# Kernel tuning notes

Hardware: AMD Instinct MI355X
Metric: run time of the kernel (lower is better)

The kernel has to match this reference:

```python
import jax, jax.numpy as jnp
import numpy as np

P = 3          # patch_length
P2 = 9         # patch_length**2
CENTER = 4     # patch_center_idx = P2 // 2
REF_LEN = 1    # reference_patch_length
EPS_SHIFT = 1e-6


def _unfold3(feat):
    # F.unfold(feat, 3, padding=1).view(B, C*9, H, W): channel order c*9 + ki*3 + kj
    B, C, H, W = feat.shape
    p = jnp.pad(feat, ((0, 0), (0, 0), (1, 1), (1, 1)))
    patches = [p[:, :, i:i + H, j:j + W] for i in range(3) for j in range(3)]
    return jnp.stack(patches, axis=2).reshape(B, C * 9, H, W)


def _mlp(x, w0, b0, w1, b1, w2, b2, w3, b3, w4, b4):
    h = jax.nn.relu(x @ w0 + b0)
    h = jax.nn.relu(h @ w1 + b1)
    h = jax.nn.relu(h @ w2 + b2)
    h = jax.nn.relu(h @ w3 + b3)
    return h @ w4 + b4


def _forward(feat, coord, cell, w0, b0, w1, b1, w2, b2, w3, b3, w4, b4):
    B, C, H, W = feat.shape
    Q = coord.shape[1]
    featu = _unfold3(feat)                      # (B, C*9, H, W)
    rx = 1.0 / H                                # 2 / H / 2
    ry = 1.0 / W
    coord_p = coord.reshape(B, Q, P2, 2)        # pairs: [...,0]=h-coord, [...,1]=w-coord
    bidx = jnp.arange(B)[:, None]
    # bug-faithful rel_coord scaling: even indices scaled by H then W, odd never
    rel_scale = jnp.array([float(H) * float(W), 1.0], coord.dtype)
    cell_scale = jnp.array([float(H), float(W)], cell.dtype)
    v_lst = [i for i in range(-REF_LEN, REF_LEN + 1) if i != 0]
    preds, areas = [], []
    for vx in v_lst:
        for vy in v_lst:
            shift = jnp.array([vx * rx + EPS_SHIFT, vy * ry + EPS_SHIFT], coord.dtype)
            center = jnp.clip(coord_p[:, :, CENTER, :] + shift, -1 + 1e-6, 1 - 1e-6)
            # nearest grid_sample, align_corners=False: idx = round((g+1)*size/2 - 0.5)
            row = jnp.clip(jnp.round((center[..., 0] + 1) * H / 2 - 0.5).astype(jnp.int32), 0, H - 1)
            col = jnp.clip(jnp.round((center[..., 1] + 1) * W / 2 - 0.5).astype(jnp.int32), 0, W - 1)
            q_feat = featu[bidx, :, row, col]                       # (B, Q, C*9)
            q_coord = jnp.stack([(2 * row + 1) / H - 1,
                                 (2 * col + 1) / W - 1], -1).astype(coord.dtype)
            rel = (coord_p - q_coord[:, :, None, :]) * rel_scale    # (B, Q, P2, 2)
            rel_flat = rel.reshape(B, Q, 2 * P2)
            rel_cell = cell * cell_scale
            x = jnp.concatenate([q_feat, rel_flat, rel_cell], axis=-1)
            pred = _mlp(x, w0, b0, w1, b1, w2, b2, w3, b3, w4, b4)  # (B, Q, 27)
            preds.append(pred)
            areas.append(jnp.abs(rel[:, :, 0, 0] * rel[:, :, 0, 1]) + 1e-9)
    tot = areas[0] + areas[1] + areas[2] + areas[3]
    # local_ensemble: swap diagonally opposite areas
    areas[0], areas[3] = areas[3], areas[0]
    areas[1], areas[2] = areas[2], areas[1]
    ret = jnp.zeros_like(preds[0])
    for p_, a_ in zip(preds, areas):
        ret = ret + p_ * (a_ / tot)[..., None]
    return ret


def setup_inputs() -> dict:
    key = jax.random.key(0)
    ks = jax.random.split(key, 8)
    B, C, H, W, Q = 8, 64, 48, 48, 8192
    HID, OUT = 256, 27
    in_dim = C * 9 + 2 * P2 + 2  # 596
    feat = jax.random.normal(ks[0], (B, C, H, W), jnp.float32)
    coord = jax.random.uniform(ks[1], (B, Q, 2 * P2), jnp.float32, -1.0, 1.0)
    cell = jnp.full((B, Q, 2), 2.0 / (H * 4), jnp.float32)

    def lin(k, fi, fo):
        return (jax.random.normal(k, (fi, fo), jnp.float32) / np.sqrt(fi)).astype(jnp.float32)

    return {
        'feat': feat, 'coord': coord, 'cell': cell,
        'w0': lin(ks[2], in_dim, HID), 'b0': jnp.zeros((HID,), jnp.float32),
        'w1': lin(ks[3], HID, HID), 'b1': jnp.zeros((HID,), jnp.float32),
        'w2': lin(ks[4], HID, HID), 'b2': jnp.zeros((HID,), jnp.float32),
        'w3': lin(ks[5], HID, HID), 'b3': jnp.zeros((HID,), jnp.float32),
        'w4': lin(ks[6], HID, OUT), 'b4': jnp.zeros((OUT,), jnp.float32),
    }


def reference(feat, coord, cell, w0, b0, w1, b1, w2, b2, w3, b3, w4, b4):
    return _forward(feat, coord, cell, w0, b0, w1, b1, w2, b2, w3, b3, w4, b4)
```

## Files before the change

### kernel.cpp

```cpp
#include <hip/hip_runtime.h>
#include <hip/hip_bf16.h>

typedef _Float16 f16x8 __attribute__((ext_vector_type(8)));
typedef float f32x4 __attribute__((ext_vector_type(4)));

#define BQ 65536
#define KPAD0 640
#define HID 256
#define NOUT 27

__device__ __forceinline__ void gl_lds16(const _Float16* g, _Float16* l) {
    __builtin_amdgcn_global_load_lds(
        (const __attribute__((address_space(1))) void*)g,
        (__attribute__((address_space(3))) void*)l, 16, 0, 0);
}

__global__ __launch_bounds__(256) void feat_transpose(
    const float* __restrict__ feat, _Float16* __restrict__ featT,
    _Float16* __restrict__ zbuf)
{
    __shared__ float tile[64 * 49];
    int bh = blockIdx.x;
    int b = bh / 48, h = bh - b * 48;
    int t = threadIdx.x;
    if (bh == 0 && t < 128) zbuf[t] = (_Float16)0.f;
    #pragma unroll
    for (int i = 0; i < 12; i++) {
        int idx = t + i * 256;
        int c = idx / 48, w = idx - c * 48;
        tile[c * 49 + w] = feat[(((size_t)b * 64 + c) * 48 + h) * 48 + w];
    }
    __syncthreads();
    #pragma unroll
    for (int i = 0; i < 12; i++) {
        int idx = t + i * 256;
        int w = idx >> 6, c = idx & 63;
        featT[(((size_t)b * 48 + h) * 48 + w) * 64 + c] = (_Float16)tile[c * 49 + w];
    }
}

__global__ void transpose_cast(const float* __restrict__ w, _Float16* __restrict__ wt,
                               int Kin, int Nin, int Kpad, int Npad) {
    int idx = blockIdx.x * 256 + threadIdx.x;
    if (idx >= Npad * Kpad) return;
    int n = idx / Kpad, k = idx - n * Kpad;
    float v = (n < Nin && k < Kin) ? w[k * Nin + n] : 0.f;
    wt[idx] = (_Float16)v;
}

__global__ void transpose_cast_w0(const float* __restrict__ w0, _Float16* __restrict__ wt) {
    int idx = blockIdx.x * 256 + threadIdx.x;
    if (idx >= 256 * KPAD0) return;
    int n = idx / KPAD0, kp = idx - n * KPAD0;
    int src = (kp < 576) ? ((kp & 63) * 9 + (kp >> 6)) : kp;
    float v = (src < 596) ? w0[src * 256 + n] : 0.f;
    wt[idx] = (_Float16)v;
}

__global__ __launch_bounds__(256, 2) void mega(
    const _Float16* __restrict__ featT, const float* __restrict__ coord,
    const float* __restrict__ cell, const _Float16* __restrict__ zbuf,
    const _Float16* __restrict__ W0t, const _Float16* __restrict__ W1t,
    const _Float16* __restrict__ W2t, const _Float16* __restrict__ W3t,
    const _Float16* __restrict__ W4t,
    const float* __restrict__ b0, const float* __restrict__ b1,
    const float* __restrict__ b2, const float* __restrict__ b3,
    const float* __restrict__ b4, float* __restrict__ preds)
{
    __shared__ _Float16 act[64 * 256];
    __shared__ _Float16 Bs[256 * 32];
    __shared__ int   rc_s[64][2];
    __shared__ float q_s[64][2];
    __shared__ float wgt[64];

    int t = threadIdx.x;
    int wave = t >> 6, lane = t & 63;
    int lrow = lane & 15, lq = lane >> 4;
    int blk = blockIdx.x;
    int s = blk & 3;
    int bq0 = (blk >> 2) * 64;
    _Float16* As = act;

    if (t < 64) {
        int bq = bq0 + t;
        const float* cp = coord + (size_t)bq * 18;
        float areas[4]; int mri = 0, mci = 0; float mqx = 0.f, mqy = 0.f;
        #pragma unroll
        for (int ss = 0; ss < 4; ss++) {
            float vx = (ss & 2) ? 1.f : -1.f, vy = (ss & 1) ? 1.f : -1.f;
            float cx = cp[8] + vx * (1.f / 48.f) + 1e-6f;
            float cy = cp[9] + vy * (1.f / 48.f) + 1e-6f;
            cx = fminf(fmaxf(cx, -1.f + 1e-6f), 1.f - 1e-6f);
            cy = fminf(fmaxf(cy, -1.f + 1e-6f), 1.f - 1e-6f);
            int ri = (int)rintf((cx + 1.f) * 24.f - 0.5f); ri = min(max(ri, 0), 47);
            int ci = (int)rintf((cy + 1.f) * 24.f - 0.5f); ci = min(max(ci, 0), 47);
            float qx = (float)(2 * ri + 1) / 48.f - 1.f;
            float qy = (float)(2 * ci + 1) / 48.f - 1.f;
            areas[ss] = fabsf((cp[0] - qx) * 2304.f * (cp[1] - qy)) + 1e-9f;
            if (ss == s) { mri = ri; mci = ci; mqx = qx; mqy = qy; }
        }
        float tot = areas[0] + areas[1] + areas[2] + areas[3];
        wgt[t] = areas[s ^ 3] / tot;
        rc_s[t][0] = mri; rc_s[t][1] = mci;
        q_s[t][0] = mqx;  q_s[t][1] = mqy;
    }
    __syncthreads();

    int gdat = (lane & 3) ^ ((lane >> 3) & 3);

    f32x4 acc[4][4];
    #pragma unroll
    for (int mi = 0; mi < 4; mi++)
        #pragma unroll
        for (int ni = 0; ni < 4; ni++) acc[mi][ni] = (f32x4){0.f, 0.f, 0.f, 0.f};

    {
        int srow = wave * 16 + (lane >> 2);
        int sbq  = bq0 + srow;
        int s_ri = rc_s[srow][0], s_ci = rc_s[srow][1];
        const _Float16* fbase = featT + ((size_t)(sbq >> 13)) * (48 * 48 * 64);

        for (int p = 0; p < 9; p++) {
            int di = p / 3 - 1, dj = p - (p / 3) * 3 - 1;
            int r2 = s_ri + di, c2 = s_ci + dj;
            const _Float16* src = ((unsigned)r2 < 48u && (unsigned)c2 < 48u)
                ? fbase + (((size_t)r2 * 48 + c2) << 6) : zbuf;
            #pragma unroll
            for (int half = 0; half < 2; half++) {
                __syncthreads();
                gl_lds16(src + half * 32 + gdat * 8, &As[wave * 512]);
                int k0 = p * 64 + half * 32;
                #pragma unroll
                for (int j = 0; j < 4; j++) {
                    int slab = j * 4 + wave;
                    int br = slab * 16 + (lane >> 2);
                    gl_lds16(W0t + (size_t)br * KPAD0 + k0 + gdat * 8, &Bs[slab * 512]);
                }
                __syncthreads();
                f16x8 af[4], bf[4];
                #pragma unroll
                for (int mi = 0; mi < 4; mi++) {
                    int ar = mi * 16 + lrow;
                    af[mi] = *(const f16x8*)&As[ar * 32 + ((lq ^ ((ar >> 1) & 3)) << 3)];
                }
                #pragma unroll
                for (int ni = 0; ni < 4; ni++) {
                    int br = wave * 64 + ni * 16 + lrow;
                    bf[ni] = *(const f16x8*)&Bs[br * 32 + ((lq ^ ((br >> 1) & 3)) << 3)];
                }
                #pragma unroll
                for (int mi = 0; mi < 4; mi++)
                    #pragma unroll
                    for (int ni = 0; ni < 4; ni++)
                        acc[mi][ni] = __builtin_amdgcn_mfma_f32_16x16x32_f16(
                            af[mi], bf[ni], acc[mi][ni], 0, 0, 0);
            }
        }
        {
            __syncthreads();
            int r = t >> 2, c0 = (t & 3) * 8;
            int bq = bq0 + r;
            const float* cp2 = coord + (size_t)bq * 18;
            float qx = q_s[r][0], qy = q_s[r][1];
            _Float16 tmp[8];
            #pragma unroll
            for (int j = 0; j < 8; j++) {
                int idx = c0 + j;
                float v;
                if (idx < 18) v = (idx & 1) ? (cp2[idx] - qy) : ((cp2[idx] - qx) * 2304.f);
                else if (idx == 18) v = cell[(size_t)bq * 2] * 48.f;
                else if (idx == 19) v = cell[(size_t)bq * 2 + 1] * 48.f;
                else v = 0.f;
                tmp[j] = (_Float16)v;
            }
            int gslot = ((c0 >> 3) ^ ((r >> 1) & 3)) & 3;
            *(int4*)&As[r * 32 + gslot * 8] = *(int4*)&tmp[0];
            #pragma unroll
            for (int j = 0; j < 4; j++) {
                int slab = j * 4 + wave;
                int br = slab * 16 + (lane >> 2);
                gl_lds16(W0t + (size_t)br * KPAD0 + 576 + gdat * 8, &Bs[slab * 512]);
            }
            __syncthreads();
            f16x8 af[4], bf[4];
            #pragma unroll
            for (int mi = 0; mi < 4; mi++) {
                int ar = mi * 16 + lrow;
                af[mi] = *(const f16x8*)&As[ar * 32 + ((lq ^ ((ar >> 1) & 3)) << 3)];
            }
            #pragma unroll
            for (int ni = 0; ni < 4; ni++) {
                int br = wave * 64 + ni * 16 + lrow;
                bf[ni] = *(const f16x8*)&Bs[br * 32 + ((lq ^ ((br >> 1) & 3)) << 3)];
            }
            #pragma unroll
            for (int mi = 0; mi < 4; mi++)
                #pragma unroll
                for (int ni = 0; ni < 4; ni++)
                    acc[mi][ni] = __builtin_amdgcn_mfma_f32_16x16x32_f16(
                        af[mi], bf[ni], acc[mi][ni], 0, 0, 0);
        }
    }
    __syncthreads();
    {
        float bvv[4];
        #pragma unroll
        for (int ni = 0; ni < 4; ni++) bvv[ni] = b0[wave * 64 + ni * 16 + lrow];
        #pragma unroll
        for (int mi = 0; mi < 4; mi++)
            #pragma unroll
            for (int ni = 0; ni < 4; ni++) {
                int cw = wave * 64 + ni * 16 + lrow;
                #pragma unroll
                for (int rr = 0; rr < 4; rr++) {
                    float v = acc[mi][ni][rr] + bvv[ni];
                    v = v > 0.f ? v : 0.f;
                    int rw = mi * 16 + lq * 4 + rr;
                    int gp = ((cw >> 3) ^ (rw & 31)) & 31;
                    act[rw * 256 + gp * 8 + (cw & 7)] = (_Float16)v;
                }
            }
    }

    for (int layer = 0; layer < 3; layer++) {
        const _Float16* Wl = (layer == 0) ? W1t : (layer == 1) ? W2t : W3t;
        const float*    bl = (layer == 0) ? b1  : (layer == 1) ? b2  : b3;
        #pragma unroll
        for (int mi = 0; mi < 4; mi++)
            #pragma unroll
            for (int ni = 0; ni < 4; ni++) acc[mi][ni] = (f32x4){0.f, 0.f, 0.f, 0.f};
        #pragma unroll 2
        for (int k0 = 0; k0 < 256; k0 += 32) {
            __syncthreads();
            #pragma unroll
            for (int j = 0; j < 4; j++) {
                int slab = j * 4 + wave;
                int br = slab * 16 + (lane >> 2);
                gl_lds16(Wl + (size_t)br * 256 + k0 + gdat * 8, &Bs[slab * 512]);
            }
            __syncthreads();
            f16x8 af[4], bf[4];
            #pragma unroll
            for (int mi = 0; mi < 4; mi++) {
                int ar = mi * 16 + lrow;
                int gp = (((k0 >> 3) + lq) ^ (ar & 31)) & 31;
                af[mi] = *(const f16x8*)&act[ar * 256 + gp * 8];
            }
            #pragma unroll
            for (int ni = 0; ni < 4; ni++) {
                int br = wave * 64 + ni * 16 + lrow;
                bf[ni] = *(const f16x8*)&Bs[br * 32 + ((lq ^ ((br >> 1) & 3)) << 3)];
            }
            #pragma unroll
            for (int mi = 0; mi < 4; mi++)
                #pragma unroll
                for (int ni = 0; ni < 4; ni++)
                    acc[mi][ni] = __builtin_amdgcn_mfma_f32_16x16x32_f16(
                        af[mi], bf[ni], acc[mi][ni], 0, 0, 0);
        }
        __syncthreads();
        {
            float bvv[4];
            #pragma unroll
            for (int ni = 0; ni < 4; ni++) bvv[ni] = bl[wave * 64 + ni * 16 + lrow];
            #pragma unroll
            for (int mi = 0; mi < 4; mi++)
                #pragma unroll
                for (int ni = 0; ni < 4; ni++) {
                    int cw = wave * 64 + ni * 16 + lrow;
                    #pragma unroll
                    for (int rr = 0; rr < 4; rr++) {
                        float v = acc[mi][ni][rr] + bvv[ni];
                        v = v > 0.f ? v : 0.f;
                        int rw = mi * 16 + lq * 4 + rr;
                        int gp = ((cw >> 3) ^ (rw & 31)) & 31;
                        act[rw * 256 + gp * 8 + (cw & 7)] = (_Float16)v;
                    }
                }
        }
    }

    f32x4 acc2[4][2];
    #pragma unroll
    for (int mi = 0; mi < 4; mi++)
        #pragma unroll
        for (int ni = 0; ni < 2; ni++) acc2[mi][ni] = (f32x4){0.f, 0.f, 0.f, 0.f};
    #pragma unroll 2
    for (int k0 = 0; k0 < 256; k0 += 32) {
        __syncthreads();
        if (wave < 2) {
            int br = wave * 16 + (lane >> 2);
            gl_lds16(W4t + (size_t)br * 256 + k0 + gdat * 8, &Bs[wave * 512]);
        }
        __syncthreads();
        if (wave == 0) {
            f16x8 af[4], bf[2];
            #pragma unroll
            for (int mi = 0; mi < 4; mi++) {
                int ar = mi * 16 + lrow;
                int gp = (((k0 >> 3) + lq) ^ (ar & 31)) & 31;
                af[mi] = *(const f16x8*)&act[ar * 256 + gp * 8];
            }
            #pragma unroll
            for (int ni = 0; ni < 2; ni++) {
                int br = ni * 16 + lrow;
                bf[ni] = *(const f16x8*)&Bs[br * 32 + ((lq ^ ((br >> 1) & 3)) << 3)];
            }
            #pragma unroll
            for (int mi = 0; mi < 4; mi++)
                #pragma unroll
                for (int ni = 0; ni < 2; ni++)
                    acc2[mi][ni] = __builtin_amdgcn_mfma_f32_16x16x32_f16(
                        af[mi], bf[ni], acc2[mi][ni], 0, 0, 0);
        }
    }

    if (wave == 0) {
        float bv0 = b4[lrow];
        float bv1 = (lrow < 11) ? b4[16 + lrow] : 0.f;
        float* pr = preds + (size_t)s * (BQ * NOUT);
        #pragma unroll
        for (int mi = 0; mi < 4; mi++)
            #pragma unroll
            for (int rr = 0; rr < 4; rr++) {
                int row = mi * 16 + lq * 4 + rr;
                float w = wgt[row];
                size_t obase = (size_t)(bq0 + row) * 27;
                pr[obase + lrow] = w * (acc2[mi][0][rr] + bv0);
                if (lrow < 11)
                    pr[obase + 16 + lrow] = w * (acc2[mi][1][rr] + bv1);
            }
    }
}

__global__ __launch_bounds__(256) void combine_kernel(
    const float* __restrict__ preds, float* __restrict__ out)
{
    int idx = blockIdx.x * 256 + threadIdx.x;
    if (idx >= BQ * NOUT) return;
    const size_t st = (size_t)BQ * NOUT;
    out[idx] = preds[idx] + preds[st + idx] + preds[2 * st + idx] + preds[3 * st + idx];
}

extern "C" void kernel_launch(void* const* d_in, const int* in_sizes, int n_in,
                              void* d_out, int out_size, void* d_ws, size_t ws_size,
                              hipStream_t stream) {
    const float* feat  = (const float*)d_in[0];
    const float* coord = (const float*)d_in[1];
    const float* cell  = (const float*)d_in[2];
    const float* w0 = (const float*)d_in[3];  const float* b0 = (const float*)d_in[4];
    const float* w1 = (const float*)d_in[5];  const float* b1 = (const float*)d_in[6];
    const float* w2 = (const float*)d_in[7];  const float* b2 = (const float*)d_in[8];
    const float* w3 = (const float*)d_in[9];  const float* b3 = (const float*)d_in[10];
    const float* w4 = (const float*)d_in[11]; const float* b4 = (const float*)d_in[12];
    float* out = (float*)d_out;

    char* ws = (char*)d_ws;
    size_t off = 0;
    _Float16* W0t = (_Float16*)(ws + off); off += (size_t)256 * KPAD0 * 2;
    _Float16* W1t = (_Float16*)(ws + off); off += (size_t)256 * 256 * 2;
    _Float16* W2t = (_Float16*)(ws + off); off += (size_t)256 * 256 * 2;
    _Float16* W3t = (_Float16*)(ws + off); off += (size_t)256 * 256 * 2;
    _Float16* W4t = (_Float16*)(ws + off); off += (size_t)32 * 256 * 2;
    _Float16* featT = (_Float16*)(ws + off); off += (size_t)8 * 48 * 48 * 64 * 2;
    _Float16* zbuf  = (_Float16*)(ws + off); off += 512;
    float* preds    = (float*)(ws + off);    off += (size_t)4 * BQ * NOUT * 4;

    feat_transpose<<<8 * 48, 256, 0, stream>>>(feat, featT, zbuf);
    transpose_cast_w0<<<(256 * KPAD0 + 255) / 256, 256, 0, stream>>>(w0, W0t);
    transpose_cast<<<256, 256, 0, stream>>>(w1, W1t, 256, 256, 256, 256);
    transpose_cast<<<256, 256, 0, stream>>>(w2, W2t, 256, 256, 256, 256);
    transpose_cast<<<256, 256, 0, stream>>>(w3, W3t, 256, 256, 256, 256);
    transpose_cast<<<32, 256, 0, stream>>>(w4, W4t, 256, NOUT, 256, 32);

    mega<<<4 * (BQ / 64), 256, 0, stream>>>(featT, coord, cell, zbuf,
                                            W0t, W1t, W2t, W3t, W4t,
                                            b0, b1, b2, b3, b4, preds);

    combine_kernel<<<(BQ * NOUT + 255) / 256, 256, 0, stream>>>(preds, out);
}
```

Measured before the change: 392.3 us.

## Load MFMA operands directly from global memory instead of staging through LDS

After: 627.0 us. 59.8% more time.

```diff
diff --git a/kernel.cpp b/kernel.cpp
--- a/kernel.cpp
+++ b/kernel.cpp
@@ -8,12 +8,7 @@
 #define KPAD0 640
 #define HID 256
 #define NOUT 27
-
-__device__ __forceinline__ void gl_lds16(const _Float16* g, _Float16* l) {
-    __builtin_amdgcn_global_load_lds(
-        (const __attribute__((address_space(1))) void*)g,
-        (__attribute__((address_space(3))) void*)l, 16, 0, 0);
-}
+#define ZOFF 1179648
 
 __global__ __launch_bounds__(256) void feat_transpose(
     const float* __restrict__ feat, _Float16* __restrict__ featT,
@@ -59,7 +54,7 @@
 
 __global__ __launch_bounds__(256, 2) void mega(
     const _Float16* __restrict__ featT, const float* __restrict__ coord,
-    const float* __restrict__ cell, const _Float16* __restrict__ zbuf,
+    const float* __restrict__ cell,
     const _Float16* __restrict__ W0t, const _Float16* __restrict__ W1t,
     const _Float16* __restrict__ W2t, const _Float16* __restrict__ W3t,
     const _Float16* __restrict__ W4t,
@@ -68,7 +63,7 @@
     const float* __restrict__ b4, float* __restrict__ preds)
 {
     __shared__ _Float16 act[64 * 256];
-    __shared__ _Float16 Bs[256 * 32];
+    __shared__ int   pixA[9 * 64];
     __shared__ int   rc_s[64][2];
     __shared__ float q_s[64][2];
     __shared__ float wgt[64];
@@ -79,7 +74,6 @@
     int blk = blockIdx.x;
     int s = blk & 3;
     int bq0 = (blk >> 2) * 64;
-    _Float16* As = act;
 
     if (t < 64) {
         int bq = bq0 + t;
@@ -105,8 +99,36 @@
         q_s[t][0] = mqx;  q_s[t][1] = mqy;
     }
     __syncthreads();
-
-    int gdat = (lane & 3) ^ ((lane >> 3) & 3);
+    {
+        int e = t;
+        if (e < 576) {
+            int p = e >> 6, row = e & 63;
+            int di = p / 3 - 1, dj = p - (p / 3) * 3 - 1;
+            int ri = rc_s[row][0] + di, ci = rc_s[row][1] + dj;
+            int b = (bq0 + row) >> 13;
+            pixA[e] = ((unsigned)ri < 48u && (unsigned)ci < 48u)
+                    ? (((b * 48 + ri) * 48 + ci) << 6) : ZOFF;
+        }
+        e = t + 256;
+        if (e < 576) {
+            int p = e >> 6, row = e & 63;
+            int di = p / 3 - 1, dj = p - (p / 3) * 3 - 1;
+            int ri = rc_s[row][0] + di, ci = rc_s[row][1] + dj;
+            int b = (bq0 + row) >> 13;
+            pixA[e] = ((unsigned)ri < 48u && (unsigned)ci < 48u)
+                    ? (((b * 48 + ri) * 48 + ci) << 6) : ZOFF;
+        }
+        e = t + 512;
+        if (e < 576) {
+            int p = e >> 6, row = e & 63;
+            int di = p / 3 - 1, dj = p - (p / 3) * 3 - 1;
+            int ri = rc_s[row][0] + di, ci = rc_s[row][1] + dj;
+            int b = (bq0 + row) >> 13;
+            pixA[e] = ((unsigned)ri < 48u && (unsigned)ci < 48u)
+                    ? (((b * 48 + ri) * 48 + ci) << 6) : ZOFF;
+        }
+    }
+    __syncthreads();
 
     f32x4 acc[4][4];
     #pragma unroll
@@ -114,58 +136,41 @@
         #pragma unroll
         for (int ni = 0; ni < 4; ni++) acc[mi][ni] = (f32x4){0.f, 0.f, 0.f, 0.f};
 
+    for (int p = 0; p < 9; p++) {
+        #pragma unroll
+        for (int half = 0; half < 2; half++) {
+            f16x8 af[4], bf[4];
+            #pragma unroll
+            for (int mi = 0; mi < 4; mi++) {
+                int off = pixA[p * 64 + mi * 16 + lrow];
+                af[mi] = *(const f16x8*)(featT + off + half * 32 + lq * 8);
+            }
+            int k0 = p * 64 + half * 32;
+            #pragma unroll
+            for (int ni = 0; ni < 4; ni++) {
+                int br = wave * 64 + ni * 16 + lrow;
+                bf[ni] = *(const f16x8*)&W0t[(size_t)br * KPAD0 + k0 + lq * 8];
+            }
+            #pragma unroll
+            for (int mi = 0; mi < 4; mi++)
+                #pragma unroll
+                for (int ni = 0; ni < 4; ni++)
+                    acc[mi][ni] = __builtin_amdgcn_mfma_f32_16x16x32_f16(
+                        af[mi], bf[ni], acc[mi][ni], 0, 0, 0);
+        }
+    }
     {
-        int srow = wave * 16 + (lane >> 2);
-        int sbq  = bq0 + srow;
-        int s_ri = rc_s[srow][0], s_ci = rc_s[srow][1];
-        const _Float16* fbase = featT + ((size_t)(sbq >> 13)) * (48 * 48 * 64);
-
-        for (int p = 0; p < 9; p++) {
-            int di = p / 3 - 1, dj = p - (p / 3) * 3 - 1;
-            int r2 = s_ri + di, c2 = s_ci + dj;
-            const _Float16* src = ((unsigned)r2 < 48u && (unsigned)c2 < 48u)
-                ? fbase + (((size_t)r2 * 48 + c2) << 6) : zbuf;
-            #pragma unroll
-            for (int half = 0; half < 2; half++) {
-                __syncthreads();
-                gl_lds16(src + half * 32 + gdat * 8, &As[wave * 512]);
-                int k0 = p * 64 + half * 32;
-                #pragma unroll
-                for (int j = 0; j < 4; j++) {
-                    int slab = j * 4 + wave;
-                    int br = slab * 16 + (lane >> 2);
-                    gl_lds16(W0t + (size_t)br * KPAD0 + k0 + gdat * 8, &Bs[slab * 512]);
-                }
-                __syncthreads();
-                f16x8 af[4], bf[4];
-                #pragma unroll
-                for (int mi = 0; mi < 4; mi++) {
-                    int ar = mi * 16 + lrow;
-                    af[mi] = *(const f16x8*)&As[ar * 32 + ((lq ^ ((ar >> 1) & 3)) << 3)];
-                }
-                #pragma unroll
-                for (int ni = 0; ni < 4; ni++) {
-                    int br = wave * 64 + ni * 16 + lrow;
-                    bf[ni] = *(const f16x8*)&Bs[br * 32 + ((lq ^ ((br >> 1) & 3)) << 3)];
-                }
-                #pragma unroll
-                for (int mi = 0; mi < 4; mi++)
-                    #pragma unroll
-                    for (int ni = 0; ni < 4; ni++)
-                        acc[mi][ni] = __builtin_amdgcn_mfma_f32_16x16x32_f16(
-                            af[mi], bf[ni], acc[mi][ni], 0, 0, 0);
-            }
-        }
-        {
-            __syncthreads();
-            int r = t >> 2, c0 = (t & 3) * 8;
-            int bq = bq0 + r;
+        f16x8 af[4], bf[4];
+        #pragma unroll
+        for (int mi = 0; mi < 4; mi++) {
+            int row = mi * 16 + lrow;
+            int bq = bq0 + row;
             const float* cp2 = coord + (size_t)bq * 18;
-            float qx = q_s[r][0], qy = q_s[r][1];
+            float qx = q_s[row][0], qy = q_s[row][1];
             _Float16 tmp[8];
             #pragma unroll
             for (int j = 0; j < 8; j++) {
-                int idx = c0 + j;
+                int idx = lq * 8 + j;
                 float v;
                 if (idx < 18) v = (idx & 1) ? (cp2[idx] - qy) : ((cp2[idx] - qx) * 2304.f);
                 else if (idx == 18) v = cell[(size_t)bq * 2] * 48.f;
@@ -173,35 +178,20 @@
                 else v = 0.f;
                 tmp[j] = (_Float16)v;
             }
-            int gslot = ((c0 >> 3) ^ ((r >> 1) & 3)) & 3;
-            *(int4*)&As[r * 32 + gslot * 8] = *(int4*)&tmp[0];
-            #pragma unroll
-            for (int j = 0; j < 4; j++) {
-                int slab = j * 4 + wave;
-                int br = slab * 16 + (lane >> 2);
-                gl_lds16(W0t + (size_t)br * KPAD0 + 576 + gdat * 8, &Bs[slab * 512]);
-            }
-            __syncthreads();
-            f16x8 af[4], bf[4];
-            #pragma unroll
-            for (int mi = 0; mi < 4; mi++) {
-                int ar = mi * 16 + lrow;
-                af[mi] = *(const f16x8*)&As[ar * 32 + ((lq ^ ((ar >> 1) & 3)) << 3)];
-            }
-            #pragma unroll
-            for (int ni = 0; ni < 4; ni++) {
-                int br = wave * 64 + ni * 16 + lrow;
-                bf[ni] = *(const f16x8*)&Bs[br * 32 + ((lq ^ ((br >> 1) & 3)) << 3)];
-            }
-            #pragma unroll
-            for (int mi = 0; mi < 4; mi++)
-                #pragma unroll
-                for (int ni = 0; ni < 4; ni++)
-                    acc[mi][ni] = __builtin_amdgcn_mfma_f32_16x16x32_f16(
-                        af[mi], bf[ni], acc[mi][ni], 0, 0, 0);
-        }
-    }
-    __syncthreads();
+            af[mi] = *(f16x8*)tmp;
+        }
+        #pragma unroll
+        for (int ni = 0; ni < 4; ni++) {
+            int br = wave * 64 + ni * 16 + lrow;
+            bf[ni] = *(const f16x8*)&W0t[(size_t)br * KPAD0 + 576 + lq * 8];
+        }
+        #pragma unroll
+        for (int mi = 0; mi < 4; mi++)
+            #pragma unroll
+            for (int ni = 0; ni < 4; ni++)
+                acc[mi][ni] = __builtin_amdgcn_mfma_f32_16x16x32_f16(
+                    af[mi], bf[ni], acc[mi][ni], 0, 0, 0);
+    }
     {
         float bvv[4];
         #pragma unroll
@@ -221,6 +211,7 @@
                 }
             }
     }
+    __syncthreads();
 
     for (int layer = 0; layer < 3; layer++) {
         const _Float16* Wl = (layer == 0) ? W1t : (layer == 1) ? W2t : W3t;
@@ -231,14 +222,6 @@
             for (int ni = 0; ni < 4; ni++) acc[mi][ni] = (f32x4){0.f, 0.f, 0.f, 0.f};
         #pragma unroll 2
         for (int k0 = 0; k0 < 256; k0 += 32) {
-            __syncthreads();
-            #pragma unroll
-            for (int j = 0; j < 4; j++) {
-                int slab = j * 4 + wave;
-                int br = slab * 16 + (lane >> 2);
-                gl_lds16(Wl + (size_t)br * 256 + k0 + gdat * 8, &Bs[slab * 512]);
-            }
-            __syncthreads();
             f16x8 af[4], bf[4];
             #pragma unroll
             for (int mi = 0; mi < 4; mi++) {
@@ -249,7 +232,7 @@
             #pragma unroll
             for (int ni = 0; ni < 4; ni++) {
                 int br = wave * 64 + ni * 16 + lrow;
-                bf[ni] = *(const f16x8*)&Bs[br * 32 + ((lq ^ ((br >> 1) & 3)) << 3)];
+                bf[ni] = *(const f16x8*)&Wl[(size_t)br * 256 + k0 + lq * 8];
             }
             #pragma unroll
             for (int mi = 0; mi < 4; mi++)
@@ -278,58 +261,44 @@
                     }
                 }
         }
-    }
-
-    f32x4 acc2[4][2];
-    #pragma unroll
-    for (int mi = 0; mi < 4; mi++)
-        #pragma unroll
-        for (int ni = 0; ni < 2; ni++) acc2[mi][ni] = (f32x4){0.f, 0.f, 0.f, 0.f};
+        __syncthreads();
+    }
+
+    f32x4 acc2[2];
+    acc2[0] = (f32x4){0.f, 0.f, 0.f, 0.f};
+    acc2[1] = (f32x4){0.f, 0.f, 0.f, 0.f};
+    int mrow0 = wave * 16;
     #pragma unroll 2
     for (int k0 = 0; k0 < 256; k0 += 32) {
-        __syncthreads();
-        if (wave < 2) {
-            int br = wave * 16 + (lane >> 2);
-            gl_lds16(W4t + (size_t)br * 256 + k0 + gdat * 8, &Bs[wave * 512]);
-        }
-        __syncthreads();
-        if (wave == 0) {
-            f16x8 af[4], bf[2];
-            #pragma unroll
-            for (int mi = 0; mi < 4; mi++) {
-                int ar = mi * 16 + lrow;
-                int gp = (((k0 >> 3) + lq) ^ (ar & 31)) & 31;
-                af[mi] = *(const f16x8*)&act[ar * 256 + gp * 8];
-            }
-            #pragma unroll
-            for (int ni = 0; ni < 2; ni++) {
-                int br = ni * 16 + lrow;
-                bf[ni] = *(const f16x8*)&Bs[br * 32 + ((lq ^ ((br >> 1) & 3)) << 3)];
-            }
-            #pragma unroll
-            for (int mi = 0; mi < 4; mi++)
-                #pragma unroll
-                for (int ni = 0; ni < 2; ni++)
-                    acc2[mi][ni] = __builtin_amdgcn_mfma_f32_16x16x32_f16(
-                        af[mi], bf[ni], acc2[mi][ni], 0, 0, 0);
-        }
-    }
-
-    if (wave == 0) {
+        f16x8 af, bf[2];
+        {
+            int ar = mrow0 + lrow;
+            int gp = (((k0 >> 3) + lq) ^ (ar & 31)) & 31;
+            af = *(const f16x8*)&act[ar * 256 + gp * 8];
+        }
+        #pragma unroll
+        for (int ni = 0; ni < 2; ni++) {
+            int br = ni * 16 + lrow;
+            bf[ni] = *(const f16x8*)&W4t[(size_t)br * 256 + k0 + lq * 8];
+        }
+        #pragma unroll
+        for (int ni = 0; ni < 2; ni++)
+            acc2[ni] = __builtin_amdgcn_mfma_f32_16x16x32_f16(af, bf[ni], acc2[ni], 0, 0, 0);
+    }
+
+    {
         float bv0 = b4[lrow];
         float bv1 = (lrow < 11) ? b4[16 + lrow] : 0.f;
         float* pr = preds + (size_t)s * (BQ * NOUT);
         #pragma unroll
-        for (int mi = 0; mi < 4; mi++)
-            #pragma unroll
-            for (int rr = 0; rr < 4; rr++) {
-                int row = mi * 16 + lq * 4 + rr;
-                float w = wgt[row];
-                size_t obase = (size_t)(bq0 + row) * 27;
-                pr[obase + lrow] = w * (acc2[mi][0][rr] + bv0);
-                if (lrow < 11)
-                    pr[obase + 16 + lrow] = w * (acc2[mi][1][rr] + bv1);
-            }
+        for (int rr = 0; rr < 4; rr++) {
+            int row = mrow0 + lq * 4 + rr;
+            float w = wgt[row];
+            size_t obase = (size_t)(bq0 + row) * 27;
+            pr[obase + lrow] = w * (acc2[0][rr] + bv0);
+            if (lrow < 11)
+                pr[obase + 16 + lrow] = w * (acc2[1][rr] + bv1);
+        }
     }
 }
 
@@ -362,7 +331,7 @@
     _Float16* W2t = (_Float16*)(ws + off); off += (size_t)256 * 256 * 2;
     _Float16* W3t = (_Float16*)(ws + off); off += (size_t)256 * 256 * 2;
     _Float16* W4t = (_Float16*)(ws + off); off += (size_t)32 * 256 * 2;
-    _Float16* featT = (_Float16*)(ws + off); off += (size_t)8 * 48 * 48 * 64 * 2;
+    _Float16* featT = (_Float16*)(ws + off); off += (size_t)ZOFF * 2;
     _Float16* zbuf  = (_Float16*)(ws + off); off += 512;
     float* preds    = (float*)(ws + off);    off += (size_t)4 * BQ * NOUT * 4;
 
@@ -373,7 +342,7 @@
     transpose_cast<<<256, 256, 0, stream>>>(w3, W3t, 256, 256, 256, 256);
     transpose_cast<<<32, 256, 0, stream>>>(w4, W4t, 256, NOUT, 256, 32);
 
-    mega<<<4 * (BQ / 64), 256, 0, stream>>>(featT, coord, cell, zbuf,
+    mega<<<4 * (BQ / 64), 256, 0, stream>>>(featT, coord, cell,
                                             W0t, W1t, W2t, W3t, W4t,
                                             b0, b1, b2, b3, b4, preds);
 
```
